# Optimization experiments

Measured on AMD Instinct MI355X. Metric: run time of the kernel, lower is better.

## Reference

```python
import jax, jax.numpy as jnp
import numpy as np

N_NODES = 100000
N_EDGES = 3200000
NUM_GRAPHS = 128
DIM = 2


def setup_inputs() -> dict:
    key = jax.random.key(0)
    k1, k2, k3 = jax.random.split(key, 3)
    node_pos = jax.random.normal(k1, (N_NODES, DIM), dtype=jnp.float32)
    raw_edge_index = jax.random.randint(k2, (2, N_EDGES), 0, N_NODES, dtype=jnp.int64)
    batch = jnp.sort(jax.random.randint(k3, (N_NODES,), 0, NUM_GRAPHS, dtype=jnp.int64))
    return {"node_pos": node_pos, "raw_edge_index": raw_edge_index, "batch": batch}


def reference(node_pos, raw_edge_index, batch):
    # gather edge endpoints: [E, DIM]
    start = node_pos[raw_edge_index[0]]
    end = node_pos[raw_edge_index[1]]
    # per-edge (||end - start|| - 1)^2 : [E]
    eu = jnp.linalg.norm(end - start, axis=1)
    edge_var = jnp.square(eu - 1.0)
    # graph id of each edge (via its source node): [E]
    index = batch[raw_edge_index[0]]
    # scatter-mean by graph
    sums = jax.ops.segment_sum(edge_var, index, num_segments=NUM_GRAPHS)
    counts = jax.ops.segment_sum(jnp.ones_like(edge_var), index, num_segments=NUM_GRAPHS)
    graph_var = sums / jnp.maximum(counts, 1.0)
    # self.reduce defaults to torch.mean over graphs -> scalar
    return jnp.mean(graph_var)
```

## Files before the change

### kernel.cpp

```cpp
#include <hip/hip_runtime.h>

#define NGRAPH 128
#define NBLK   1024
#define BS     256

#define FIX_SCALE 262144.0f
#define CNT_SHIFT 42


__global__ __launch_bounds__(BS) void edgevar_pack(
    const float2* __restrict__ pos,
    const int*    __restrict__ batch,
    float4*       __restrict__ packed,
    int N) {
  const int i = blockIdx.x * BS + threadIdx.x;
  if (i < N) {
    float2 p = pos[i];
    packed[i] = make_float4(p.x, p.y, __int_as_float(batch[i]), 0.f);
  }
}

__global__ __launch_bounds__(BS) void edgevar_stage1(
    const float4* __restrict__ packed,
    const int*    __restrict__ ei,
    unsigned long long* __restrict__ part,
    int E) {
  __shared__ unsigned long long s_acc[4][NGRAPH];
  {
    unsigned long long* f = &s_acc[0][0];
    if (threadIdx.x < 2 * NGRAPH) {
      f[threadIdx.x] = 0ull;
      f[threadIdx.x + 2 * NGRAPH] = 0ull;
    }
  }
  __syncthreads();

  const int cp  = threadIdx.x & 3;
  const int tid = blockIdx.x * BS + threadIdx.x;
  const int nth = NBLK * BS;
  const int E4  = E >> 2;
  const int4*   __restrict__ s4  = (const int4*)ei;
  const int4*   __restrict__ d4  = (const int4*)(ei + E);
  const float2* __restrict__ pp2 = (const float2*)packed;

  for (int i = tid; i < E4; i += nth) {
    int4 s = s4[i];
    int4 d = d4[i];
    int ss[4] = {s.x, s.y, s.z, s.w};
    int dd[4] = {d.x, d.y, d.z, d.w};
#pragma unroll
    for (int k = 0; k < 4; ++k) {
      float4 a = packed[ss[k]];
      float2 b = pp2[2 * dd[k]];
      float dx = b.x - a.x, dy = b.y - a.y;
      float v  = sqrtf(dx * dx + dy * dy) - 1.f;
      v *= v;
      int g = __float_as_int(a.z);
      unsigned long long contrib =
          (1ull << CNT_SHIFT) | (unsigned long long)(v * FIX_SCALE + 0.5f);
      atomicAdd(&s_acc[cp][g], contrib);
    }
  }
  for (int e = (E4 << 2) + tid; e < E; e += nth) {
    float4 a = packed[ei[e]];
    float2 b = pp2[2 * ei[e + E]];
    float dx = b.x - a.x, dy = b.y - a.y;
    float v  = sqrtf(dx * dx + dy * dy) - 1.f;
    v *= v;
    int g = __float_as_int(a.z);
    unsigned long long contrib =
        (1ull << CNT_SHIFT) | (unsigned long long)(v * FIX_SCALE + 0.5f);
    atomicAdd(&s_acc[cp][g], contrib);
  }

  __syncthreads();
  if (threadIdx.x < NGRAPH) {
    unsigned long long t = s_acc[0][threadIdx.x] + s_acc[1][threadIdx.x]
                         + s_acc[2][threadIdx.x] + s_acc[3][threadIdx.x];
    part[(size_t)blockIdx.x * NGRAPH + threadIdx.x] = t;
  }
}

__global__ __launch_bounds__(1024) void edgevar_stage2(
    const unsigned long long* __restrict__ part,
    float* __restrict__ out) {
  const int t    = threadIdx.x;
  const int slot = t & (NGRAPH - 1);
  const int rc   = t >> 7;
  const int ROWS = NBLK / 8;

  unsigned long long acc = 0ull;
  const unsigned long long* p = part + (size_t)rc * ROWS * NGRAPH + slot;
#pragma unroll 8
  for (int r = 0; r < ROWS; ++r) acc += p[(size_t)r * NGRAPH];

  __shared__ unsigned long long s[1024];
  s[t] = acc;
  __syncthreads();

  __shared__ float var[NGRAPH];
  if (t < NGRAPH) {
    unsigned long long tot = 0ull;
#pragma unroll
    for (int j = 0; j < 8; ++j) tot += s[t + NGRAPH * j];
    unsigned int       cnt = (unsigned int)(tot >> CNT_SHIFT);
    unsigned long long fx  = tot & ((1ull << CNT_SHIFT) - 1ull);
    float sum = (float)fx * (1.0f / FIX_SCALE);
    var[t] = sum / fmaxf((float)cnt, 1.f);
  }
  __syncthreads();

  if (t < 64) {
    float v = var[t] + var[t + 64];
    for (int off = 32; off; off >>= 1) v += __shfl_down(v, off);
    if (t == 0) out[0] = v * (1.0f / NGRAPH);
  }
}

extern "C" void kernel_launch(void* const* d_in, const int* in_sizes, int n_in,
                              void* d_out, int out_size, void* d_ws, size_t ws_size,
                              hipStream_t stream) {
  const float2* pos   = (const float2*)d_in[0];
  const int*    ei    = (const int*)d_in[1];
  const int*    batch = (const int*)d_in[2];
  float*        out   = (float*)d_out;
  const int N = in_sizes[0] / 2;
  const int E = in_sizes[1] / 2;

  float4*             packed = (float4*)d_ws;
  unsigned long long* part   =
      (unsigned long long*)((char*)d_ws + (size_t)N * sizeof(float4));

  hipLaunchKernelGGL(edgevar_pack, dim3((N + BS - 1) / BS), dim3(BS), 0, stream,
                     pos, batch, packed, N);
  hipLaunchKernelGGL(edgevar_stage1, dim3(NBLK), dim3(BS), 0, stream,
                     packed, ei, part, E);
  hipLaunchKernelGGL(edgevar_stage2, dim3(1), dim3(1024), 0, stream,
                     part, out);
}
```

Before: 116.0 us.

## Parallelize final reduction across graphs with transposed partials and more blocks

Doubles the stage-1 grid and stores per-block partial sums transposed (graph-major), so the second stage can run one block per graph and read coalesced rows instead of a single 1024-thread block reducing everything. A new tiny third kernel averages the per-graph variances. This removes the serial single-block reduction bottleneck but adds one extra kernel launch, twice as many partials, and strided writes from stage 1.

```diff
diff --git a/kernel.cpp b/kernel.cpp
--- a/kernel.cpp
+++ b/kernel.cpp
@@ -1,7 +1,7 @@
 #include <hip/hip_runtime.h>
 
 #define NGRAPH 128
-#define NBLK   1024
+#define NBLK   2048
 #define BS     256
 
 #define FIX_SCALE 262144.0f
@@ -77,44 +77,38 @@
   if (threadIdx.x < NGRAPH) {
     unsigned long long t = s_acc[0][threadIdx.x] + s_acc[1][threadIdx.x]
                          + s_acc[2][threadIdx.x] + s_acc[3][threadIdx.x];
-    part[(size_t)blockIdx.x * NGRAPH + threadIdx.x] = t;
+    part[(size_t)threadIdx.x * NBLK + blockIdx.x] = t;
   }
 }
 
-__global__ __launch_bounds__(1024) void edgevar_stage2(
+__global__ __launch_bounds__(BS) void edgevar_stage2(
     const unsigned long long* __restrict__ part,
-    float* __restrict__ out) {
-  const int t    = threadIdx.x;
-  const int slot = t & (NGRAPH - 1);
-  const int rc   = t >> 7;
-  const int ROWS = NBLK / 8;
+    float* __restrict__ gvar) {
+  const int g = blockIdx.x;
+  const int t = threadIdx.x;
+  const unsigned long long* row = part + (size_t)g * NBLK;
+  unsigned long long acc = 0ull;
+#pragma unroll
+  for (int k = 0; k < NBLK / BS; ++k) acc += row[t + k * BS];
+  for (int off = 32; off; off >>= 1) acc += __shfl_down(acc, off);
+  __shared__ unsigned long long wsum[4];
+  if ((t & 63) == 0) wsum[t >> 6] = acc;
+  __syncthreads();
+  if (t == 0) {
+    unsigned long long tot = wsum[0] + wsum[1] + wsum[2] + wsum[3];
+    unsigned int       cnt = (unsigned int)(tot >> CNT_SHIFT);
+    float sum = (float)(tot & ((1ull << CNT_SHIFT) - 1ull)) * (1.0f / FIX_SCALE);
+    gvar[g] = sum / fmaxf((float)cnt, 1.f);
+  }
+}
 
-  unsigned long long acc = 0ull;
-  const unsigned long long* p = part + (size_t)rc * ROWS * NGRAPH + slot;
-#pragma unroll 8
-  for (int r = 0; r < ROWS; ++r) acc += p[(size_t)r * NGRAPH];
-
-  __shared__ unsigned long long s[1024];
-  s[t] = acc;
-  __syncthreads();
-
-  __shared__ float var[NGRAPH];
-  if (t < NGRAPH) {
-    unsigned long long tot = 0ull;
-#pragma unroll
-    for (int j = 0; j < 8; ++j) tot += s[t + NGRAPH * j];
-    unsigned int       cnt = (unsigned int)(tot >> CNT_SHIFT);
-    unsigned long long fx  = tot & ((1ull << CNT_SHIFT) - 1ull);
-    float sum = (float)fx * (1.0f / FIX_SCALE);
-    var[t] = sum / fmaxf((float)cnt, 1.f);
-  }
-  __syncthreads();
-
-  if (t < 64) {
-    float v = var[t] + var[t + 64];
-    for (int off = 32; off; off >>= 1) v += __shfl_down(v, off);
-    if (t == 0) out[0] = v * (1.0f / NGRAPH);
-  }
+__global__ __launch_bounds__(64) void edgevar_stage3(
+    const float* __restrict__ gvar,
+    float*       __restrict__ out) {
+  const int t = threadIdx.x;
+  float v = gvar[t] + gvar[t + 64];
+  for (int off = 32; off; off >>= 1) v += __shfl_down(v, off);
+  if (t == 0) out[0] = v * (1.0f / NGRAPH);
 }
 
 extern "C" void kernel_launch(void* const* d_in, const int* in_sizes, int n_in,
@@ -130,11 +124,14 @@
   float4*             packed = (float4*)d_ws;
   unsigned long long* part   =
       (unsigned long long*)((char*)d_ws + (size_t)N * sizeof(float4));
+  float* gvar = (float*)((char*)part + (size_t)NGRAPH * NBLK * sizeof(unsigned long long));
 
   hipLaunchKernelGGL(edgevar_pack, dim3((N + BS - 1) / BS), dim3(BS), 0, stream,
                      pos, batch, packed, N);
   hipLaunchKernelGGL(edgevar_stage1, dim3(NBLK), dim3(BS), 0, stream,
                      packed, ei, part, E);
-  hipLaunchKernelGGL(edgevar_stage2, dim3(1), dim3(1024), 0, stream,
-                     part, out);
+  hipLaunchKernelGGL(edgevar_stage2, dim3(NGRAPH), dim3(BS), 0, stream,
+                     part, gvar);
+  hipLaunchKernelGGL(edgevar_stage3, dim3(1), dim3(64), 0, stream,
+                     gvar, out);
 }
```

Measured after the change: 105.4 us. 9.2% less time.
